# Kernel tuning notes

Hardware: AMD Instinct MI355X
Metric: run time of the kernel (lower is better)

The kernel has to match this reference:

```python
import jax, jax.numpy as jnp
import numpy as np

Q_DIM = 2048
HEADS = 16
HEAD_DIM = 128
INNER = HEADS * HEAD_DIM          # 2048
MLP_HID = int(Q_DIM * 4.0)        # 8192
MLP_MULT = 2
EPS = 1e-05
B, S = 2, 2048


def setup_inputs() -> dict:
    key = jax.random.key(0)
    ks = jax.random.split(key, 4)
    hidden_states = jax.random.normal(ks[0], (B, S, Q_DIM), dtype=jnp.float32)
    # interleaved RoPE tables: cos/sin of shape [S, HEAD_DIM]
    half = HEAD_DIM // 2
    freqs = 1.0 / (10000.0 ** (np.arange(half, dtype=np.float64) / half))
    ang = np.outer(np.arange(S, dtype=np.float64), freqs)      # [S, half]
    ang = np.repeat(ang, 2, axis=-1)                            # [S, HEAD_DIM]
    rope_cos = jnp.asarray(np.cos(ang), dtype=jnp.float32)
    rope_sin = jnp.asarray(np.sin(ang), dtype=jnp.float32)
    fused_out = 3 * INNER + MLP_HID * MLP_MULT                  # 22528
    W_qkv_mlp = jax.random.normal(ks[1], (Q_DIM, fused_out), dtype=jnp.float32) * (Q_DIM ** -0.5)
    norm_q_w = jnp.ones((HEAD_DIM,), dtype=jnp.float32)
    norm_k_w = jnp.ones((HEAD_DIM,), dtype=jnp.float32)
    W_out = jax.random.normal(ks[2], (INNER + MLP_HID, Q_DIM), dtype=jnp.float32) * ((INNER + MLP_HID) ** -0.5)
    b_out = jnp.zeros((Q_DIM,), dtype=jnp.float32)
    return {"hidden_states": hidden_states, "rope_cos": rope_cos, "rope_sin": rope_sin,
            "W_qkv_mlp": W_qkv_mlp, "norm_q_w": norm_q_w, "norm_k_w": norm_k_w,
            "W_out": W_out, "b_out": b_out}


def _rms_norm(x, w):
    # RMSNorm over the last (head_dim) axis
    return x * jax.lax.rsqrt(jnp.mean(x * x, axis=-1, keepdims=True) + EPS) * w


def _apply_rope(x, cos, sin):
    # x: [B, S, H, D]; interleaved rotate-half (diffusers real-rope convention)
    xr = x.reshape(*x.shape[:-1], HEAD_DIM // 2, 2)
    rot = jnp.stack([-xr[..., 1], xr[..., 0]], axis=-1).reshape(x.shape)
    return x * cos[None, :, None, :] + rot * sin[None, :, None, :]


def reference(hidden_states, rope_cos, rope_sin, W_qkv_mlp, norm_q_w, norm_k_w, W_out, b_out):
    b, s, _ = hidden_states.shape
    proj = hidden_states @ W_qkv_mlp                              # [B,S,22528]
    qkv, mlp_h = jnp.split(proj, [3 * INNER], axis=-1)
    q, k, v = jnp.split(qkv, 3, axis=-1)
    q = q.reshape(b, s, HEADS, HEAD_DIM)
    k = k.reshape(b, s, HEADS, HEAD_DIM)
    v = v.reshape(b, s, HEADS, HEAD_DIM)
    q = _rms_norm(q, norm_q_w)
    k = _rms_norm(k, norm_k_w)
    q = _apply_rope(q, rope_cos, rope_sin)
    k = _apply_rope(k, rope_cos, rope_sin)
    scale = HEAD_DIM ** -0.5
    scores = jnp.einsum('bqhd,bkhd->bhqk', q, k) * scale          # [B,H,S,S]
    attn = jax.nn.softmax(scores, axis=-1)
    out_attn = jnp.einsum('bhqk,bkhd->bqhd', attn, v).reshape(b, s, INNER)
    m1, m2 = jnp.split(mlp_h, 2, axis=-1)                         # SwiGLU
    mlp_out = jax.nn.silu(m1) * m2                                # [B,S,MLP_HID]
    cat = jnp.concatenate([out_attn, mlp_out], axis=-1)           # [B,S,INNER+MLP_HID]
    return cat @ W_out + b_out
```

## Files before the change

kernel.cpp:

```cpp
#include <hip/hip_runtime.h>

typedef unsigned short u16;
typedef unsigned int u32;
typedef __bf16 bf16x8 __attribute__((ext_vector_type(8)));
typedef float f32x4 __attribute__((ext_vector_type(4)));

#define MFMA16(a, b, c) __builtin_amdgcn_mfma_f32_16x16x32_bf16((a), (b), (c), 0, 0, 0)

#define S_LEN 2048
#define D_HEAD 128
#define NHEADS 16
#define NBH 32
#define QDIM 2048
#define NPROJ 22528
#define NCAT 10240
#define MROWS 4096

#define BARRIER() __builtin_amdgcn_s_barrier()
#define SCHEDB() __builtin_amdgcn_sched_barrier(0)
#define WAITLGKM() asm volatile("s_waitcnt lgkmcnt(0)" ::: "memory")
#define WAITVM8() asm volatile("s_waitcnt vmcnt(8)" ::: "memory")
#define WAITVM0() asm volatile("s_waitcnt vmcnt(0)" ::: "memory")

__device__ __forceinline__ float bf2f(u16 u) { return __uint_as_float(((u32)u) << 16); }
__device__ __forceinline__ u16 f2bf(float f) {
  u32 u = __float_as_uint(f);
  return (u16)((u + 0x7FFFu + ((u >> 16) & 1u)) >> 16);
}
__device__ __forceinline__ void gld16(const void* g, void* l) {
  __builtin_amdgcn_global_load_lds((__attribute__((address_space(1))) void*)(g),
                                   (__attribute__((address_space(3))) void*)(l), 16, 0, 0);
}

__global__ __launch_bounds__(256) void f32_to_bf16(const float* __restrict__ in,
                                                   u16* __restrict__ out) {
  const u32 i = blockIdx.x * 256 + threadIdx.x;
  const float4 v = ((const float4*)in)[i];
  uint2 o;
  o.x = (u32)f2bf(v.x) | ((u32)f2bf(v.y) << 16);
  o.y = (u32)f2bf(v.z) | ((u32)f2bf(v.w) << 16);
  ((uint2*)out)[i] = o;
}

__global__ __launch_bounds__(256) void transpose_f32_bf16(const float* __restrict__ in,
                                                          u16* __restrict__ out, int R, int C) {
  __shared__ u16 tile[64][65];
  const int tx = threadIdx.x & 63;
  const int ty = threadIdx.x >> 6;
  const int c0 = blockIdx.x * 64;
  const int r0 = blockIdx.y * 64;
#pragma unroll
  for (int it = 0; it < 16; ++it) {
    const int rr = ty * 16 + it;
    tile[rr][tx] = f2bf(in[(size_t)(r0 + rr) * C + c0 + tx]);
  }
  __syncthreads();
#pragma unroll
  for (int it = 0; it < 16; ++it) {
    const int rr = ty * 16 + it;
    out[(size_t)(c0 + rr) * R + r0 + tx] = tile[tx][rr];
  }
}

__global__ __launch_bounds__(256) void transpose_bf16_b(const u16* __restrict__ in,
                                                        u16* __restrict__ out, int R, int C) {
  __shared__ u16 tile[64][65];
  const int z = blockIdx.z;
  in += (size_t)z * R * C;
  out += (size_t)z * R * C;
  const int tx = threadIdx.x & 63;
  const int ty = threadIdx.x >> 6;
  const int c0 = blockIdx.x * 64;
  const int r0 = blockIdx.y * 64;
#pragma unroll
  for (int it = 0; it < 16; ++it) {
    const int rr = ty * 16 + it;
    tile[rr][tx] = in[(size_t)(r0 + rr) * C + c0 + tx];
  }
  __syncthreads();
#pragma unroll
  for (int it = 0; it < 16; ++it) {
    const int rr = ty * 16 + it;
    out[(size_t)(c0 + rr) * R + r0 + tx] = tile[tx][rr];
  }
}


__device__ __forceinline__ void stage_tile(const u16* __restrict__ src, int ldk,
                                           u16* ldsbase, int k0, int t) {
  const int w64 = t & ~63;
#pragma unroll
  for (int j = 0; j < 4; ++j) {
    const int o = (j * 512 + t) * 16;
    const int row = o >> 7;
    const int g = (o & 127) >> 4;
    const int gs = g ^ (row & 7);
    gld16(src + (size_t)row * ldk + k0 + gs * 8, ldsbase + (((j * 512 + w64) * 16) >> 1));
  }
}

__device__ __forceinline__ bf16x8 rdfrag(const u16* lds, int row, int kc, int lg) {
  return *(const bf16x8*)&lds[row * 64 + (((kc * 4 + lg) ^ (row & 7)) << 3)];
}

__global__ __launch_bounds__(512, 2) void gemm256(const u16* __restrict__ A,
                                                  const u16* __restrict__ Bt,
                                                  u16* __restrict__ C, int N, int K,
                                                  int nbm) {
  __shared__ u16 As[2][256 * 64];
  __shared__ u16 Bs[2][256 * 64];
  const int t = threadIdx.x;
  const int l = t & 63;
  const int w = t >> 6;
  const int lr = l & 15;
  const int lg = l >> 4;
  const int wm = (w >> 2) * 128;
  const int wn = (w & 3) * 64;

  const int nwg = gridDim.x;
  const int cpx = nwg >> 3;
  const int swz = (blockIdx.x & 7) * cpx + (blockIdx.x >> 3);
  const int bm = swz % nbm;
  const int bn = swz / nbm;
  const u16* Ab = A + (size_t)(bm * 256) * K;
  const u16* Bb = Bt + (size_t)(bn * 256) * K;
  const int NT = K >> 6;

  f32x4 acc[8][4] = {};

  stage_tile(Bb, K, &Bs[0][0], 0, t);
  stage_tile(Ab, K, &As[0][0], 0, t);
  stage_tile(Bb, K, &Bs[1][0], 64, t);
  stage_tile(Ab, K, &As[1][0], 64, t);
  WAITVM8();
  BARRIER();

  for (int kt = 0; kt < NT; ++kt) {
    const int d = kt & 1;
    const u16* Al = &As[d][0];
    const u16* Bl = &Bs[d][0];
    const bool pre = (kt + 2 < NT);
    bf16x8 a_[4][2], b01[2][2], b23[2][2];

#pragma unroll
    for (int i = 0; i < 4; ++i)
#pragma unroll
      for (int kc = 0; kc < 2; ++kc) a_[i][kc] = rdfrag(Al, wm + i * 16 + lr, kc, lg);
#pragma unroll
    for (int j = 0; j < 2; ++j)
#pragma unroll
      for (int kc = 0; kc < 2; ++kc) b01[j][kc] = rdfrag(Bl, wn + j * 16 + lr, kc, lg);
    BARRIER();
    SCHEDB();
    WAITLGKM();
    __builtin_amdgcn_s_setprio(1);
#pragma unroll
    for (int kc = 0; kc < 2; ++kc)
#pragma unroll
      for (int i = 0; i < 4; ++i)
#pragma unroll
        for (int j = 0; j < 2; ++j) acc[i][j] = MFMA16(a_[i][kc], b01[j][kc], acc[i][j]);
    __builtin_amdgcn_s_setprio(0);
    SCHEDB();
    BARRIER();

#pragma unroll
    for (int j = 0; j < 2; ++j)
#pragma unroll
      for (int kc = 0; kc < 2; ++kc) b23[j][kc] = rdfrag(Bl, wn + 32 + j * 16 + lr, kc, lg);
    BARRIER();
    SCHEDB();
    WAITLGKM();
    __builtin_amdgcn_s_setprio(1);
#pragma unroll
    for (int kc = 0; kc < 2; ++kc)
#pragma unroll
      for (int i = 0; i < 4; ++i)
#pragma unroll
        for (int j = 0; j < 2; ++j)
          acc[i][2 + j] = MFMA16(a_[i][kc], b23[j][kc], acc[i][2 + j]);
    __builtin_amdgcn_s_setprio(0);
    SCHEDB();
    BARRIER();

#pragma unroll
    for (int i = 0; i < 4; ++i)
#pragma unroll
      for (int kc = 0; kc < 2; ++kc) a_[i][kc] = rdfrag(Al, wm + 64 + i * 16 + lr, kc, lg);
    if (pre) stage_tile(Bb, K, &Bs[d][0], (kt + 2) * 64, t);
    BARRIER();
    SCHEDB();
    WAITLGKM();
    __builtin_amdgcn_s_setprio(1);
#pragma unroll
    for (int kc = 0; kc < 2; ++kc)
#pragma unroll
      for (int i = 0; i < 4; ++i)
#pragma unroll
        for (int j = 0; j < 2; ++j)
          acc[4 + i][2 + j] = MFMA16(a_[i][kc], b23[j][kc], acc[4 + i][2 + j]);
    __builtin_amdgcn_s_setprio(0);
    SCHEDB();
    BARRIER();

    if (pre) stage_tile(Ab, K, &As[d][0], (kt + 2) * 64, t);
    BARRIER();
    SCHEDB();
    __builtin_amdgcn_s_setprio(1);
#pragma unroll
    for (int kc = 0; kc < 2; ++kc)
#pragma unroll
      for (int i = 0; i < 4; ++i)
#pragma unroll
        for (int j = 0; j < 2; ++j)
          acc[4 + i][j] = MFMA16(a_[i][kc], b01[j][kc], acc[4 + i][j]);
    __builtin_amdgcn_s_setprio(0);
    SCHEDB();
    if (pre) {
      WAITVM8();
    } else {
      WAITVM0();
    }
    BARRIER();
  }

  const int m0 = bm * 256 + wm;
  const int n0 = bn * 256 + wn;
#pragma unroll
  for (int i = 0; i < 8; ++i)
#pragma unroll
    for (int j = 0; j < 4; ++j)
#pragma unroll
      for (int r = 0; r < 4; ++r) {
        const int row = m0 + i * 16 + lg * 4 + r;
        const int col = n0 + j * 16 + lr;
        C[(size_t)row * N + col] = f2bf(acc[i][j][r]);
      }
}

template <int OUTF32>
__global__ __launch_bounds__(256, 2) void gemm_bt(const u16* __restrict__ A,
                                                  const u16* __restrict__ Bt,
                                                  void* __restrict__ Cvoid,
                                                  const float* __restrict__ bias, int N, int K,
                                                  int nbn) {
  __shared__ u16 As[128 * 64];
  __shared__ u16 Bs[128 * 64];
  const int t = threadIdx.x;
  const int l = t & 63;
  const int w = t >> 6;
  const int lr = l & 15;
  const int lg = l >> 4;
  const int nwg = gridDim.x;
  const int cpx = nwg >> 3;
  const int swz = (blockIdx.x & 7) * cpx + (blockIdx.x >> 3);
  const int bm = swz / nbn;
  const int bn = swz % nbn;
  const int m0 = bm * 128;
  const int n0 = bn * 128;
  const int wm = (w >> 1) * 64;
  const int wn = (w & 1) * 64;

  f32x4 acc[4][4] = {};
  const int obase = w * 1024 + l * 16;

  for (int k0 = 0; k0 < K; k0 += 64) {
#pragma unroll
    for (int rnd = 0; rnd < 4; ++rnd) {
      const int o = obase + rnd * 4096;
      const int row = o >> 7;
      const int g = (o & 127) >> 4;
      const int gs = g ^ (row & 7);
      gld16(A + (size_t)(m0 + row) * K + k0 + gs * 8, &As[rnd * 2048 + w * 512]);
      gld16(Bt + (size_t)(n0 + row) * K + k0 + gs * 8, &Bs[rnd * 2048 + w * 512]);
    }
    __syncthreads();

    bf16x8 af[4][2], bfr[4][2];
#pragma unroll
    for (int i = 0; i < 4; ++i) {
#pragma unroll
      for (int kc = 0; kc < 2; ++kc) {
        const int ra = wm + i * 16 + lr;
        af[i][kc] = *(const bf16x8*)&As[ra * 64 + (((kc * 4 + lg) ^ (ra & 7)) * 8)];
        const int rb = wn + i * 16 + lr;
        bfr[i][kc] = *(const bf16x8*)&Bs[rb * 64 + (((kc * 4 + lg) ^ (rb & 7)) * 8)];
      }
    }
#pragma unroll
    for (int kc = 0; kc < 2; ++kc)
#pragma unroll
      for (int i = 0; i < 4; ++i)
#pragma unroll
        for (int j = 0; j < 4; ++j)
          acc[i][j] = MFMA16(af[i][kc], bfr[j][kc], acc[i][j]);
    __syncthreads();
  }

  if (OUTF32) {
    float* C = (float*)Cvoid;
#pragma unroll
    for (int i = 0; i < 4; ++i)
#pragma unroll
      for (int j = 0; j < 4; ++j)
#pragma unroll
        for (int r = 0; r < 4; ++r) {
          const int row = m0 + wm + i * 16 + lg * 4 + r;
          const int col = n0 + wn + j * 16 + lr;
          C[(size_t)row * N + col] = acc[i][j][r] + bias[col];
        }
  } else {
    u16* C = (u16*)Cvoid;
#pragma unroll
    for (int i = 0; i < 4; ++i)
#pragma unroll
      for (int j = 0; j < 4; ++j)
#pragma unroll
        for (int r = 0; r < 4; ++r) {
          const int row = m0 + wm + i * 16 + lg * 4 + r;
          const int col = n0 + wn + j * 16 + lr;
          C[(size_t)row * N + col] = f2bf(acc[i][j][r]);
        }
  }
}

__global__ __launch_bounds__(256) void norm_rope(const u16* __restrict__ proj,
                                                 const float* __restrict__ cosT,
                                                 const float* __restrict__ sinT,
                                                 const float* __restrict__ wq,
                                                 const float* __restrict__ wk,
                                                 u16* __restrict__ Qb, u16* __restrict__ Kb,
                                                 u16* __restrict__ Vb) {
  const int l = threadIdx.x & 63;
  const int wg = blockIdx.x * 4 + (threadIdx.x >> 6);
  const int h = wg & 15;
  const int r = wg >> 4;
  const int b = r >> 11;
  const int s = r & 2047;
  const int bh = (b << 4) + h;

  const u16* p = proj + (size_t)r * NPROJ + h * 128 + 2 * l;
  const u32 qu = *(const u32*)(p);
  const u32 ku = *(const u32*)(p + QDIM);
  const u32 vu = *(const u32*)(p + 2 * QDIM);

  const float q0 = bf2f(qu & 0xffff), q1 = bf2f(qu >> 16);
  const float k0 = bf2f(ku & 0xffff), k1 = bf2f(ku >> 16);

  float sq = q0 * q0 + q1 * q1;
  float sk = k0 * k0 + k1 * k1;
#pragma unroll
  for (int m = 1; m < 64; m <<= 1) {
    sq += __shfl_xor(sq, m);
    sk += __shfl_xor(sk, m);
  }
  const float scq = rsqrtf(sq * (1.0f / 128.0f) + 1e-5f);
  const float sck = rsqrtf(sk * (1.0f / 128.0f) + 1e-5f);

  const float2 cc = *(const float2*)&cosT[s * 128 + 2 * l];
  const float2 ssn = *(const float2*)&sinT[s * 128 + 2 * l];
  const float w0 = wq[2 * l], w1 = wq[2 * l + 1];
  const float x0 = wk[2 * l], x1 = wk[2 * l + 1];

  const float qn0 = q0 * scq * w0, qn1 = q1 * scq * w1;
  const float kn0 = k0 * sck * x0, kn1 = k1 * sck * x1;

  const float ATT = 0.08838834764831845f;
  const float qr0 = (qn0 * cc.x - qn1 * ssn.x) * ATT;
  const float qr1 = (qn1 * cc.y + qn0 * ssn.y) * ATT;
  const float kr0 = kn0 * cc.x - kn1 * ssn.x;
  const float kr1 = kn1 * cc.y + kn0 * ssn.y;

  const size_t dst = ((size_t)bh * S_LEN + s) * 128 + 2 * l;
  *(u32*)(Qb + dst) = (u32)f2bf(qr0) | ((u32)f2bf(qr1) << 16);
  *(u32*)(Kb + dst) = (u32)f2bf(kr0) | ((u32)f2bf(kr1) << 16);
  *(u32*)(Vb + dst) = vu;
}

__global__ __launch_bounds__(256) void swiglu(const u16* __restrict__ proj,
                                              u16* __restrict__ Cat) {
  const u32 i = blockIdx.x * 256 + threadIdx.x;
  const u32 r = i >> 11;
  const u32 c = (i & 2047) * 4;
  const u16* p1 = proj + (size_t)r * NPROJ + 3 * QDIM + c;
  const uint2 a = *(const uint2*)p1;
  const uint2 bv = *(const uint2*)(p1 + 8192);
  const float a0 = bf2f(a.x & 0xffff), a1 = bf2f(a.x >> 16);
  const float a2 = bf2f(a.y & 0xffff), a3 = bf2f(a.y >> 16);
  const float b0 = bf2f(bv.x & 0xffff), b1 = bf2f(bv.x >> 16);
  const float b2 = bf2f(bv.y & 0xffff), b3 = bf2f(bv.y >> 16);
  const float o0 = a0 / (1.f + __expf(-a0)) * b0;
  const float o1 = a1 / (1.f + __expf(-a1)) * b1;
  const float o2 = a2 / (1.f + __expf(-a2)) * b2;
  const float o3 = a3 / (1.f + __expf(-a3)) * b3;
  uint2 o;
  o.x = (u32)f2bf(o0) | ((u32)f2bf(o1) << 16);
  o.y = (u32)f2bf(o2) | ((u32)f2bf(o3) << 16);
  *(uint2*)(Cat + (size_t)r * NCAT + QDIM + c) = o;
}

__global__ __launch_bounds__(256, 2) void attn_fwd(const u16* __restrict__ Qb,
                                                   const u16* __restrict__ Kb,
                                                   const u16* __restrict__ Vt,
                                                   u16* __restrict__ Cat) {
  __shared__ u16 Ks[64 * 128];
  __shared__ u16 Vs[128 * 64];
  __shared__ u16 Ps[4][32 * 64];

  const int t = threadIdx.x;
  const int l = t & 63;
  const int w = t >> 6;
  const int lr = l & 15;
  const int lg = l >> 4;
  const int qt = blockIdx.x;
  const int bh = blockIdx.y;
  const int b = bh >> 4;
  const int h = bh & 15;
  const int q0 = qt * 128 + w * 32;

  bf16x8 qf[2][4];
#pragma unroll
  for (int im = 0; im < 2; ++im)
#pragma unroll
    for (int kc = 0; kc < 4; ++kc)
      qf[im][kc] =
          *(const bf16x8*)&Qb[((size_t)bh * S_LEN + q0 + im * 16 + lr) * 128 + kc * 32 + lg * 8];

  f32x4 oacc[2][8] = {};
  float mrun[2][4], lrun[2][4];
#pragma unroll
  for (int im = 0; im < 2; ++im)
#pragma unroll
    for (int r = 0; r < 4; ++r) {
      mrun[im][r] = -1e30f;
      lrun[im][r] = 0.f;
    }

  const int obase = w * 1024 + l * 16;
  u16* P = Ps[w];

  for (int kt = 0; kt < 32; ++kt) {
    const int kk0 = kt * 64;
#pragma unroll
    for (int rnd = 0; rnd < 4; ++rnd) {
      const int o = obase + rnd * 4096;
      {
        const int key = o >> 8;
        const int g = (o & 255) >> 4;
        const int gs = g ^ (key & 7);
        gld16(Kb + ((size_t)bh * S_LEN + kk0 + key) * 128 + gs * 8, &Ks[rnd * 2048 + w * 512]);
      }
      {
        const int d = o >> 7;
        const int g = (o & 127) >> 4;
        const int gs = g ^ (d & 7);
        gld16(Vt + ((size_t)bh * 128 + d) * S_LEN + kk0 + gs * 8, &Vs[rnd * 2048 + w * 512]);
      }
    }
    __syncthreads();

    f32x4 sf[2][4] = {};
#pragma unroll
    for (int j = 0; j < 4; ++j) {
      const int kr = j * 16 + lr;
      bf16x8 kf[4];
#pragma unroll
      for (int kc = 0; kc < 4; ++kc)
        kf[kc] = *(const bf16x8*)&Ks[kr * 128 + (((kc * 4 + lg) ^ (kr & 7)) * 8)];
#pragma unroll
      for (int kc = 0; kc < 4; ++kc)
#pragma unroll
        for (int im = 0; im < 2; ++im)
          sf[im][j] = MFMA16(qf[im][kc], kf[kc], sf[im][j]);
    }

#pragma unroll
    for (int im = 0; im < 2; ++im) {
#pragma unroll
      for (int r = 0; r < 4; ++r) {
        float v = fmaxf(fmaxf(sf[im][0][r], sf[im][1][r]), fmaxf(sf[im][2][r], sf[im][3][r]));
        v = fmaxf(v, __shfl_xor(v, 1));
        v = fmaxf(v, __shfl_xor(v, 2));
        v = fmaxf(v, __shfl_xor(v, 4));
        v = fmaxf(v, __shfl_xor(v, 8));
        const float mnew = fmaxf(mrun[im][r], v);
        const float alpha = __expf(mrun[im][r] - mnew);
        mrun[im][r] = mnew;
        float psum = 0.f;
#pragma unroll
        for (int j = 0; j < 4; ++j) {
          const float pv = __expf(sf[im][j][r] - mnew);
          sf[im][j][r] = pv;
          psum += pv;
        }
        psum += __shfl_xor(psum, 1);
        psum += __shfl_xor(psum, 2);
        psum += __shfl_xor(psum, 4);
        psum += __shfl_xor(psum, 8);
        lrun[im][r] = lrun[im][r] * alpha + psum;
#pragma unroll
        for (int df = 0; df < 8; ++df) oacc[im][df][r] *= alpha;
      }
    }

#pragma unroll
    for (int im = 0; im < 2; ++im)
#pragma unroll
      for (int j = 0; j < 4; ++j)
#pragma unroll
        for (int r = 0; r < 4; ++r) {
          const int q = im * 16 + lg * 4 + r;
          const int key = j * 16 + lr;
          const int g = key >> 3;
          P[q * 64 + ((g ^ (q & 7)) * 8) + (key & 7)] = f2bf(sf[im][j][r]);
        }

#pragma unroll
    for (int kc = 0; kc < 2; ++kc) {
      bf16x8 pa[2];
#pragma unroll
      for (int im = 0; im < 2; ++im) {
        const int q = im * 16 + lr;
        pa[im] = *(const bf16x8*)&P[q * 64 + (((kc * 4 + lg) ^ (q & 7)) * 8)];
      }
#pragma unroll
      for (int df = 0; df < 8; ++df) {
        const int d = df * 16 + lr;
        const bf16x8 vb = *(const bf16x8*)&Vs[d * 64 + (((kc * 4 + lg) ^ (d & 7)) * 8)];
#pragma unroll
        for (int im = 0; im < 2; ++im) oacc[im][df] = MFMA16(pa[im], vb, oacc[im][df]);
      }
    }
    __syncthreads();
  }

#pragma unroll
  for (int im = 0; im < 2; ++im)
#pragma unroll
    for (int r = 0; r < 4; ++r) {
      const float inv = 1.0f / lrun[im][r];
      const int row = b * S_LEN + q0 + im * 16 + lg * 4 + r;
#pragma unroll
      for (int df = 0; df < 8; ++df) {
        const int col = h * 128 + df * 16 + lr;
        Cat[(size_t)row * NCAT + col] = f2bf(oacc[im][df][r] * inv);
      }
    }
}

extern "C" void kernel_launch(void* const* d_in, const int* in_sizes, int n_in, void* d_out,
                              int out_size, void* d_ws, size_t ws_size, hipStream_t stream) {
  (void)in_sizes; (void)n_in; (void)out_size; (void)ws_size;
  const float* hs = (const float*)d_in[0];
  const float* rcos = (const float*)d_in[1];
  const float* rsin = (const float*)d_in[2];
  const float* Wqkv = (const float*)d_in[3];
  const float* wq = (const float*)d_in[4];
  const float* wk = (const float*)d_in[5];
  const float* Wout = (const float*)d_in[6];
  const float* bout = (const float*)d_in[7];
  float* out = (float*)d_out;

  char* ws = (char*)d_ws;
  size_t off = 0;
  auto nxt = [&](size_t bytes) {
    char* p = ws + off;
    off += (bytes + 255) & ~(size_t)255;
    return p;
  };
  u16* Xb = (u16*)nxt((size_t)MROWS * QDIM * 2);
  u16* Wqkvt = (u16*)nxt((size_t)NPROJ * QDIM * 2);
  u16* Woutt = (u16*)nxt((size_t)QDIM * NCAT * 2);
  u16* proj = (u16*)nxt((size_t)MROWS * NPROJ * 2);
  u16* Qb = (u16*)nxt((size_t)NBH * S_LEN * D_HEAD * 2);
  u16* Kb = (u16*)nxt((size_t)NBH * S_LEN * D_HEAD * 2);
  u16* Vb = (u16*)nxt((size_t)NBH * S_LEN * D_HEAD * 2);
  u16* Vt = (u16*)nxt((size_t)NBH * S_LEN * D_HEAD * 2);
  u16* Cat = (u16*)nxt((size_t)MROWS * NCAT * 2);

  f32_to_bf16<<<(MROWS * QDIM / 4) / 256, 256, 0, stream>>>(hs, Xb);
  transpose_f32_bf16<<<dim3(NPROJ / 64, QDIM / 64), 256, 0, stream>>>(Wqkv, Wqkvt, QDIM, NPROJ);
  transpose_f32_bf16<<<dim3(QDIM / 64, NCAT / 64), 256, 0, stream>>>(Wout, Woutt, NCAT, QDIM);

  gemm256<<<(MROWS / 256) * (NPROJ / 256), 512, 0, stream>>>(Xb, Wqkvt, proj, NPROJ, QDIM,
                                                             MROWS / 256);

  norm_rope<<<MROWS * NHEADS / 4, 256, 0, stream>>>(proj, rcos, rsin, wq, wk, Qb, Kb, Vb);
  transpose_bf16_b<<<dim3(D_HEAD / 64, S_LEN / 64, NBH), 256, 0, stream>>>(Vb, Vt, S_LEN, D_HEAD);

  swiglu<<<(MROWS * 8192 / 4) / 256, 256, 0, stream>>>(proj, Cat);

  attn_fwd<<<dim3(S_LEN / 128, NBH), 256, 0, stream>>>(Qb, Kb, Vt, Cat);

  gemm_bt<1><<<(MROWS / 128) * (QDIM / 128), 256, 0, stream>>>(Cat, Woutt, out, bout, QDIM,
                                                               NCAT, QDIM / 128);
}
```

Baseline: 943.9 us.

## Software-pipeline LDS fragment loads across k-halves and tiles in gemm256

Restructures the gemm256 main loop so LDS fragment reads for the next MFMA cluster are issued while the current cluster runs, including prefetching the next tile's first k-half at the end of each iteration. This cuts the barriers per k-tile from seven to two and loosens the vmcnt wait from 8 to 4 to match the new global-load ordering. The aim is to hide LDS latency and remove synchronization stalls. In exchange it uses more live fragment registers and depends on a subtle ordering of buffer reuse against the async global-to-LDS stages.

```diff
diff --git a/kernel.cpp b/kernel.cpp
--- a/kernel.cpp
+++ b/kernel.cpp
@@ -20,6 +20,7 @@
 #define SCHEDB() __builtin_amdgcn_sched_barrier(0)
 #define WAITLGKM() asm volatile("s_waitcnt lgkmcnt(0)" ::: "memory")
 #define WAITVM8() asm volatile("s_waitcnt vmcnt(8)" ::: "memory")
+#define WAITVM4() asm volatile("s_waitcnt vmcnt(4)" ::: "memory")
 #define WAITVM0() asm volatile("s_waitcnt vmcnt(0)" ::: "memory")
 
 __device__ __forceinline__ float bf2f(u16 u) { return __uint_as_float(((u32)u) << 16); }
@@ -102,6 +103,14 @@
 __device__ __forceinline__ bf16x8 rdfrag(const u16* lds, int row, int kc, int lg) {
   return *(const bf16x8*)&lds[row * 64 + (((kc * 4 + lg) ^ (row & 7)) << 3)];
 }
+
+#define CLUSTER(AR, AF, BF)                                            \
+  __builtin_amdgcn_s_setprio(1);                                       \
+  _Pragma("unroll") for (int i = 0; i < 4; ++i)                        \
+  _Pragma("unroll") for (int j = 0; j < 4; ++j)                        \
+      acc[(AR) + i][j] = MFMA16(AF[i], BF[j], acc[(AR) + i][j]);       \
+  __builtin_amdgcn_s_setprio(0);                                       \
+  SCHEDB();
 
 __global__ __launch_bounds__(512, 2) void gemm256(const u16* __restrict__ A,
                                                   const u16* __restrict__ Bt,
@@ -127,6 +136,7 @@
   const int NT = K >> 6;
 
   f32x4 acc[8][4] = {};
+  bf16x8 aA[4], aB[4], bA[4], bB[4];
 
   stage_tile(Bb, K, &Bs[0][0], 0, t);
   stage_tile(Ab, K, &As[0][0], 0, t);
@@ -134,94 +144,51 @@
   stage_tile(Ab, K, &As[1][0], 64, t);
   WAITVM8();
   BARRIER();
+#pragma unroll
+  for (int i = 0; i < 4; ++i) aA[i] = rdfrag(&As[0][0], wm + i * 16 + lr, 0, lg);
+#pragma unroll
+  for (int j = 0; j < 4; ++j) bA[j] = rdfrag(&Bs[0][0], wn + j * 16 + lr, 0, lg);
 
   for (int kt = 0; kt < NT; ++kt) {
     const int d = kt & 1;
     const u16* Al = &As[d][0];
     const u16* Bl = &Bs[d][0];
+    const u16* An = &As[d ^ 1][0];
+    const u16* Bn = &Bs[d ^ 1][0];
     const bool pre = (kt + 2 < NT);
-    bf16x8 a_[4][2], b01[2][2], b23[2][2];
-
-#pragma unroll
-    for (int i = 0; i < 4; ++i)
-#pragma unroll
-      for (int kc = 0; kc < 2; ++kc) a_[i][kc] = rdfrag(Al, wm + i * 16 + lr, kc, lg);
-#pragma unroll
-    for (int j = 0; j < 2; ++j)
-#pragma unroll
-      for (int kc = 0; kc < 2; ++kc) b01[j][kc] = rdfrag(Bl, wn + j * 16 + lr, kc, lg);
+
+#pragma unroll
+    for (int i = 0; i < 4; ++i) aB[i] = rdfrag(Al, wm + 64 + i * 16 + lr, 0, lg);
+    CLUSTER(0, aA, bA)
+
+#pragma unroll
+    for (int i = 0; i < 4; ++i) aA[i] = rdfrag(Al, wm + i * 16 + lr, 1, lg);
+#pragma unroll
+    for (int j = 0; j < 4; ++j) bB[j] = rdfrag(Bl, wn + j * 16 + lr, 1, lg);
+    CLUSTER(4, aB, bA)
+    WAITLGKM();
     BARRIER();
-    SCHEDB();
+
+    if (pre) stage_tile(Bb, K, &Bs[d][0], (kt + 2) * 64, t);
+#pragma unroll
+    for (int i = 0; i < 4; ++i) aB[i] = rdfrag(Al, wm + 64 + i * 16 + lr, 1, lg);
+    CLUSTER(0, aA, bB)
     WAITLGKM();
-    __builtin_amdgcn_s_setprio(1);
-#pragma unroll
-    for (int kc = 0; kc < 2; ++kc)
-#pragma unroll
-      for (int i = 0; i < 4; ++i)
-#pragma unroll
-        for (int j = 0; j < 2; ++j) acc[i][j] = MFMA16(a_[i][kc], b01[j][kc], acc[i][j]);
-    __builtin_amdgcn_s_setprio(0);
-    SCHEDB();
-    BARRIER();
-
-#pragma unroll
-    for (int j = 0; j < 2; ++j)
-#pragma unroll
-      for (int kc = 0; kc < 2; ++kc) b23[j][kc] = rdfrag(Bl, wn + 32 + j * 16 + lr, kc, lg);
-    BARRIER();
-    SCHEDB();
-    WAITLGKM();
-    __builtin_amdgcn_s_setprio(1);
-#pragma unroll
-    for (int kc = 0; kc < 2; ++kc)
-#pragma unroll
-      for (int i = 0; i < 4; ++i)
-#pragma unroll
-        for (int j = 0; j < 2; ++j)
-          acc[i][2 + j] = MFMA16(a_[i][kc], b23[j][kc], acc[i][2 + j]);
-    __builtin_amdgcn_s_setprio(0);
-    SCHEDB();
-    BARRIER();
-
-#pragma unroll
-    for (int i = 0; i < 4; ++i)
-#pragma unroll
-      for (int kc = 0; kc < 2; ++kc) a_[i][kc] = rdfrag(Al, wm + 64 + i * 16 + lr, kc, lg);
-    if (pre) stage_tile(Bb, K, &Bs[d][0], (kt + 2) * 64, t);
-    BARRIER();
-    SCHEDB();
-    WAITLGKM();
-    __builtin_amdgcn_s_setprio(1);
-#pragma unroll
-    for (int kc = 0; kc < 2; ++kc)
-#pragma unroll
-      for (int i = 0; i < 4; ++i)
-#pragma unroll
-        for (int j = 0; j < 2; ++j)
-          acc[4 + i][2 + j] = MFMA16(a_[i][kc], b23[j][kc], acc[4 + i][2 + j]);
-    __builtin_amdgcn_s_setprio(0);
-    SCHEDB();
-    BARRIER();
-
-    if (pre) stage_tile(Ab, K, &As[d][0], (kt + 2) * 64, t);
-    BARRIER();
-    SCHEDB();
-    __builtin_amdgcn_s_setprio(1);
-#pragma unroll
-    for (int kc = 0; kc < 2; ++kc)
-#pragma unroll
-      for (int i = 0; i < 4; ++i)
-#pragma unroll
-        for (int j = 0; j < 2; ++j)
-          acc[4 + i][j] = MFMA16(a_[i][kc], b01[j][kc], acc[4 + i][j]);
-    __builtin_amdgcn_s_setprio(0);
-    SCHEDB();
     if (pre) {
-      WAITVM8();
+      WAITVM4();
     } else {
       WAITVM0();
     }
     BARRIER();
+
+    if (pre) stage_tile(Ab, K, &As[d][0], (kt + 2) * 64, t);
+    if (kt + 1 < NT) {
+#pragma unroll
+      for (int i = 0; i < 4; ++i) aA[i] = rdfrag(An, wm + i * 16 + lr, 0, lg);
+#pragma unroll
+      for (int j = 0; j < 4; ++j) bA[j] = rdfrag(Bn, wn + j * 16 + lr, 0, lg);
+    }
+    CLUSTER(4, aB, bB)
   }
 
   const int m0 = bm * 256 + wm;
```

New measurement: 1.054 ms. 11.6% more time.
